# Performance work log

Hardware: AMD Instinct MI355X
Metric: run time of the kernel (lower is better)

Reference implementation:

```python
import jax, jax.numpy as jnp
import numpy as np

B, DEC, ENC, H = 4, 128, 512, 768


def setup_inputs() -> dict:
    key = jax.random.key(0)
    k1, k2, k3, k4, k5 = jax.random.split(key, 5)
    scale = 1.0 / np.sqrt(H)
    return {
        "decoder_state": jax.random.normal(k1, (B, DEC, H), dtype=jnp.float32),
        "encoder_outputs": jax.random.normal(k2, (B, ENC, H), dtype=jnp.float32),
        "mask": jnp.zeros((B, DEC, ENC), dtype=jnp.float32),
        # Learned params: torch nn.Linear(H, H, bias=False) weights, stored as (in, out)
        "W1": jax.random.normal(k3, (H, H), dtype=jnp.float32) * scale,
        "W2": jax.random.normal(k4, (H, H), dtype=jnp.float32) * scale,
        "vt": jax.random.normal(k5, (H,), dtype=jnp.float32) * scale,
    }


def reference(decoder_state, encoder_outputs, mask, W1, W2, vt):
    # enc_t: (B, enc, H), dec_t: (B, dec, H)
    enc_t = jnp.einsum("beh,hk->bek", encoder_outputs, W1)
    dec_t = jnp.einsum("bdh,hk->bdk", decoder_state, W2)
    # Bahdanau additive score: tanh of broadcast sum -> (B, dec, enc, H), reduce with vt
    hidden = jnp.tanh(enc_t[:, None, :, :] + dec_t[:, :, None, :])
    log_score = jnp.einsum("bdek,k->bde", hidden, vt)
    log_score_masked = log_score + mask
    return (log_score_masked, log_score)
```

## Files before the change

kernel.cpp:

```cpp
#include <hip/hip_runtime.h>
#include <hip/hip_bf16.h>

#define B_SZ   4
#define DEC_SZ 128
#define ENC_SZ 512
#define H_SZ   768
#define OUT_N  (B_SZ * DEC_SZ * ENC_SZ)

typedef __attribute__((ext_vector_type(8))) short s8v;
typedef __attribute__((ext_vector_type(4))) float fvec4;

__device__ inline unsigned short f2bf(float x) {
  union { float f; unsigned u; } v; v.f = x;
  unsigned r = v.u + 0x7FFF + ((v.u >> 16) & 1);
  return (unsigned short)(r >> 16);
}

__global__ __launch_bounds__(256) void transpose_w(const float* __restrict__ W1,
                                                   const float* __restrict__ W2,
                                                   unsigned short* __restrict__ T1,
                                                   unsigned short* __restrict__ T2) {
  const float* W = blockIdx.z ? W2 : W1;
  unsigned short* T = blockIdx.z ? T2 : T1;
  __shared__ float tile[64][65];
  int c0 = blockIdx.x * 64;
  int r0 = blockIdx.y * 64;
  int tx = threadIdx.x & 63, ty = threadIdx.x >> 6;
#pragma unroll
  for (int i = 0; i < 16; ++i) {
    int r = ty + i * 4;
    tile[r][tx] = W[(size_t)(r0 + r) * H_SZ + c0 + tx];
  }
  __syncthreads();
#pragma unroll
  for (int i = 0; i < 16; ++i) {
    int c = ty + i * 4;
    T[(size_t)(c0 + c) * H_SZ + r0 + tx] = f2bf(tile[tx][c]);
  }
}

__global__ __launch_bounds__(256) void cast_bf16(const float* __restrict__ enc,
                                                 const float* __restrict__ dec,
                                                 unsigned short* __restrict__ encB,
                                                 unsigned short* __restrict__ decB) {
  const float* x = blockIdx.z ? dec : enc;
  unsigned short* y = blockIdx.z ? decB : encB;
  int n4 = blockIdx.z ? (B_SZ * DEC_SZ * H_SZ / 4) : (B_SZ * ENC_SZ * H_SZ / 4);
  int i = blockIdx.x * 256 + threadIdx.x;
  if (i >= n4) return;
  float4 v = ((const float4*)x)[i];
  ushort4 o;
  o.x = f2bf(v.x); o.y = f2bf(v.y); o.z = f2bf(v.z); o.w = f2bf(v.w);
  ((ushort4*)y)[i] = o;
}

template <int TM, bool TILED>
__global__ __launch_bounds__(256) void gemm_nt_exp(const unsigned short* __restrict__ A,
                                                   const unsigned short* __restrict__ Bm,
                                                   float* __restrict__ C, int ldc) {
  const int m0 = blockIdx.x * TM;
  const int n0 = blockIdx.y * 64;

  __shared__ unsigned short As[TM][40];
  __shared__ unsigned short Bs[64][40];

  const int tid  = threadIdx.x;
  const int wave = tid >> 6;
  const int lane = tid & 63;
  const int l16  = lane & 15;
  const int quad = lane >> 4;
  const int MI   = TM / 64;
  const int wm   = wave * (TM / 4);

  const int ASEG = TM * 4 / 256;
  int ar[2], ak[2];
#pragma unroll
  for (int i = 0; i < ASEG; ++i) {
    int seg = tid + 256 * i;
    ar[i] = seg >> 2; ak[i] = (seg & 3) * 8;
  }
  const int br = tid >> 2, bk = (tid & 3) * 8;

  fvec4 acc[2][4];
#pragma unroll
  for (int i = 0; i < 2; ++i)
#pragma unroll
    for (int j = 0; j < 4; ++j) acc[i][j] = (fvec4)0.f;

  s8v pa[2], pb;
#pragma unroll
  for (int i = 0; i < ASEG; ++i)
    pa[i] = *(const s8v*)(A + (size_t)(m0 + ar[i]) * H_SZ + ak[i]);
  pb = *(const s8v*)(Bm + (size_t)(n0 + br) * H_SZ + bk);

  for (int k0 = 0; k0 < H_SZ; k0 += 32) {
    __syncthreads();
#pragma unroll
    for (int i = 0; i < ASEG; ++i) *(s8v*)&As[ar[i]][ak[i]] = pa[i];
    *(s8v*)&Bs[br][bk] = pb;
    __syncthreads();

    if (k0 + 32 < H_SZ) {
#pragma unroll
      for (int i = 0; i < ASEG; ++i)
        pa[i] = *(const s8v*)(A + (size_t)(m0 + ar[i]) * H_SZ + k0 + 32 + ak[i]);
      pb = *(const s8v*)(Bm + (size_t)(n0 + br) * H_SZ + k0 + 32 + bk);
    }

    s8v af[2], bf[4];
#pragma unroll
    for (int i = 0; i < MI; ++i) af[i] = *(const s8v*)&As[wm + i * 16 + l16][quad * 8];
#pragma unroll
    for (int j = 0; j < 4; ++j) bf[j] = *(const s8v*)&Bs[j * 16 + l16][quad * 8];
#pragma unroll
    for (int i = 0; i < MI; ++i)
#pragma unroll
      for (int j = 0; j < 4; ++j)
        acc[i][j] = __builtin_amdgcn_mfma_f32_16x16x32_bf16(af[i], bf[j], acc[i][j], 0, 0, 0);
  }

  const float C2 = 2.885390082f;
#pragma unroll
  for (int i = 0; i < MI; ++i) {
    int mbase = m0 + wm + i * 16 + quad * 4;
#pragma unroll
    for (int j = 0; j < 4; ++j) {
      int n = n0 + j * 16 + l16;
      if (TILED) {
        float4 o;
        o.x = __builtin_amdgcn_exp2f(acc[i][j][0] * C2);
        o.y = __builtin_amdgcn_exp2f(acc[i][j][1] * C2);
        o.z = __builtin_amdgcn_exp2f(acc[i][j][2] * C2);
        o.w = __builtin_amdgcn_exp2f(acc[i][j][3] * C2);
        int bIdx = n >> 9, es = (n >> 6) & 7, el = n & 63;
        ((float4*)C)[((size_t)(bIdx * 8 + es) * 192 + (mbase >> 2)) * 64 + el] = o;
      } else {
#pragma unroll
        for (int r = 0; r < 4; ++r)
          C[(size_t)(mbase + r) * ldc + n] = __builtin_amdgcn_exp2f(acc[i][j][r] * C2);
      }
    }
  }
}

__global__ __launch_bounds__(256) void score_out(const float* __restrict__ peT,
                                                 const float* __restrict__ pdm,
                                                 const float* __restrict__ vt,
                                                 const float* __restrict__ mask,
                                                 float* __restrict__ out) {
  const int tid  = threadIdx.x;
  const int wave = tid >> 6;
  const int lane = tid & 63;
  const int es   = blockIdx.x;
  const int d0   = blockIdx.y * 8;
  const int b    = blockIdx.z;

  __shared__ float pd_s[8][776];
  __shared__ float vts[768];

  {
    const int d = tid >> 5, l = tid & 31;
    const float* row = pdm + (size_t)(b * DEC_SZ + d0 + d) * H_SZ;
#pragma unroll
    for (int i = 0; i < 6; ++i)
      *(float4*)&pd_s[d][l * 4 + i * 128] = *(const float4*)(row + l * 4 + i * 128);
  }
  if (tid < 192) *(float4*)&vts[tid * 4] = *(const float4*)(vt + tid * 4);
  __syncthreads();

  float sumv = 0.f;
#pragma unroll
  for (int j = 0; j < 12; ++j) sumv += vts[lane + 64 * j];
#pragma unroll
  for (int s = 1; s < 64; s <<= 1) sumv += __shfl_xor(sumv, s, 64);

  float t0 = 0.f, t1 = 0.f;
  const float4* pe4 = (const float4*)peT + (size_t)(b * 8 + es) * 192 * 64 + lane;

  float4 buf[4];
#pragma unroll
  for (int i = 0; i < 4; ++i) buf[i] = pe4[(size_t)i * 64];

#pragma unroll 4
  for (int c = 0; c < 192; ++c) {
    float4 cur = buf[c & 3];
    if (c + 4 < 192) buf[c & 3] = pe4[(size_t)(c + 4) * 64];
    float4 v4 = *(const float4*)&vts[c * 4];
    float4 p0 = *(const float4*)&pd_s[wave * 2 + 0][c * 4];
    float4 p1 = *(const float4*)&pd_s[wave * 2 + 1][c * 4];
    t0 = fmaf(v4.x, __builtin_amdgcn_rcpf(fmaf(cur.x, p0.x, 1.f)), t0);
    t0 = fmaf(v4.y, __builtin_amdgcn_rcpf(fmaf(cur.y, p0.y, 1.f)), t0);
    t0 = fmaf(v4.z, __builtin_amdgcn_rcpf(fmaf(cur.z, p0.z, 1.f)), t0);
    t0 = fmaf(v4.w, __builtin_amdgcn_rcpf(fmaf(cur.w, p0.w, 1.f)), t0);
    t1 = fmaf(v4.x, __builtin_amdgcn_rcpf(fmaf(cur.x, p1.x, 1.f)), t1);
    t1 = fmaf(v4.y, __builtin_amdgcn_rcpf(fmaf(cur.y, p1.y, 1.f)), t1);
    t1 = fmaf(v4.z, __builtin_amdgcn_rcpf(fmaf(cur.z, p1.z, 1.f)), t1);
    t1 = fmaf(v4.w, __builtin_amdgcn_rcpf(fmaf(cur.w, p1.w, 1.f)), t1);
  }

  const int e = es * 64 + lane;
#pragma unroll
  for (int dd = 0; dd < 2; ++dd) {
    int d = d0 + wave * 2 + dd;
    size_t idx = ((size_t)(b * DEC_SZ + d)) * ENC_SZ + e;
    float s = fmaf(-2.f, dd ? t1 : t0, sumv);
    out[idx] = s + mask[idx];
    out[OUT_N + idx] = s;
  }
}

extern "C" void kernel_launch(void* const* d_in, const int* in_sizes, int n_in,
                              void* d_out, int out_size, void* d_ws, size_t ws_size,
                              hipStream_t stream) {
  (void)in_sizes; (void)n_in; (void)out_size; (void)ws_size;
  const float* dec  = (const float*)d_in[0];
  const float* enc  = (const float*)d_in[1];
  const float* mask = (const float*)d_in[2];
  const float* W1   = (const float*)d_in[3];
  const float* W2   = (const float*)d_in[4];
  const float* vt   = (const float*)d_in[5];
  float* out = (float*)d_out;

  float* peT = (float*)d_ws;
  float* pdm = peT + (size_t)H_SZ * B_SZ * ENC_SZ;
  unsigned short* W1T  = (unsigned short*)(pdm + (size_t)B_SZ * DEC_SZ * H_SZ);
  unsigned short* W2T  = W1T + (size_t)H_SZ * H_SZ;
  unsigned short* encB = W2T + (size_t)H_SZ * H_SZ;
  unsigned short* decB = encB + (size_t)B_SZ * ENC_SZ * H_SZ;

  transpose_w<<<dim3(12, 12, 2), 256, 0, stream>>>(W1, W2, W1T, W2T);
  cast_bf16<<<dim3(B_SZ * ENC_SZ * H_SZ / 4 / 256, 1, 2), 256, 0, stream>>>(
      enc, dec, encB, decB);

  gemm_nt_exp<128, true><<<dim3(H_SZ / 128, B_SZ * ENC_SZ / 64), 256, 0, stream>>>(
      W1T, encB, peT, 0);
  gemm_nt_exp<64, false><<<dim3(B_SZ * DEC_SZ / 64, H_SZ / 64), 256, 0, stream>>>(
      decB, W2T, pdm, H_SZ);

  score_out<<<dim3(ENC_SZ / 64, DEC_SZ / 8, B_SZ), 256, 0, stream>>>(
      peT, pdm, vt, mask, out);
}
```

Baseline: 142.5 us.

## Fuse bf16 casts into GEMM loads, merge both GEMMs, simplify score kernel

Removes the separate cast_bf16 kernel by converting fp32 encoder/decoder inputs to bf16 inside the GEMM global loads. Both projection GEMMs are merged into one launch with a block-index split, and the second GEMM now uses 128-row tiles. The score kernel drops LDS staging of the decoder row and vt, reading them directly from global memory (broadcast across the wave), handles one decoder row per wave, and deepens the peT prefetch to 8. This cuts launches and intermediate traffic, at the cost of more global reads per wave and less reuse of each peT load in the score loop.

```diff
diff --git a/kernel.cpp b/kernel.cpp
--- a/kernel.cpp
+++ b/kernel.cpp
@@ -14,6 +14,15 @@
   union { float f; unsigned u; } v; v.f = x;
   unsigned r = v.u + 0x7FFF + ((v.u >> 16) & 1);
   return (unsigned short)(r >> 16);
+}
+
+__device__ inline s8v load8(const unsigned short* p) { return *(const s8v*)p; }
+__device__ inline s8v load8(const float* p) {
+  float4 a = ((const float4*)p)[0];
+  float4 b = ((const float4*)p)[1];
+  unsigned short r[8] = {f2bf(a.x), f2bf(a.y), f2bf(a.z), f2bf(a.w),
+                         f2bf(b.x), f2bf(b.y), f2bf(b.z), f2bf(b.w)};
+  return *(const s8v*)r;
 }
 
 __global__ __launch_bounds__(256) void transpose_w(const float* __restrict__ W1,
@@ -39,29 +48,13 @@
   }
 }
 
-__global__ __launch_bounds__(256) void cast_bf16(const float* __restrict__ enc,
-                                                 const float* __restrict__ dec,
-                                                 unsigned short* __restrict__ encB,
-                                                 unsigned short* __restrict__ decB) {
-  const float* x = blockIdx.z ? dec : enc;
-  unsigned short* y = blockIdx.z ? decB : encB;
-  int n4 = blockIdx.z ? (B_SZ * DEC_SZ * H_SZ / 4) : (B_SZ * ENC_SZ * H_SZ / 4);
-  int i = blockIdx.x * 256 + threadIdx.x;
-  if (i >= n4) return;
-  float4 v = ((const float4*)x)[i];
-  ushort4 o;
-  o.x = f2bf(v.x); o.y = f2bf(v.y); o.z = f2bf(v.z); o.w = f2bf(v.w);
-  ((ushort4*)y)[i] = o;
-}
-
-template <int TM, bool TILED>
-__global__ __launch_bounds__(256) void gemm_nt_exp(const unsigned short* __restrict__ A,
-                                                   const unsigned short* __restrict__ Bm,
-                                                   float* __restrict__ C, int ldc) {
-  const int m0 = blockIdx.x * TM;
-  const int n0 = blockIdx.y * 64;
-
-  __shared__ unsigned short As[TM][40];
+template <bool TILED, typename TA, typename TB>
+__device__ inline void gemm_body(const TA* __restrict__ A, const TB* __restrict__ B,
+                                 float* __restrict__ C, int ldc, int bx, int by) {
+  const int m0 = bx * 128;
+  const int n0 = by * 64;
+
+  __shared__ unsigned short As[128][40];
   __shared__ unsigned short Bs[64][40];
 
   const int tid  = threadIdx.x;
@@ -69,13 +62,11 @@
   const int lane = tid & 63;
   const int l16  = lane & 15;
   const int quad = lane >> 4;
-  const int MI   = TM / 64;
-  const int wm   = wave * (TM / 4);
-
-  const int ASEG = TM * 4 / 256;
+  const int wm   = wave * 32;
+
   int ar[2], ak[2];
 #pragma unroll
-  for (int i = 0; i < ASEG; ++i) {
+  for (int i = 0; i < 2; ++i) {
     int seg = tid + 256 * i;
     ar[i] = seg >> 2; ak[i] = (seg & 3) * 8;
   }
@@ -89,31 +80,30 @@
 
   s8v pa[2], pb;
 #pragma unroll
-  for (int i = 0; i < ASEG; ++i)
-    pa[i] = *(const s8v*)(A + (size_t)(m0 + ar[i]) * H_SZ + ak[i]);
-  pb = *(const s8v*)(Bm + (size_t)(n0 + br) * H_SZ + bk);
+  for (int i = 0; i < 2; ++i) pa[i] = load8(A + (size_t)(m0 + ar[i]) * H_SZ + ak[i]);
+  pb = load8(B + (size_t)(n0 + br) * H_SZ + bk);
 
   for (int k0 = 0; k0 < H_SZ; k0 += 32) {
     __syncthreads();
 #pragma unroll
-    for (int i = 0; i < ASEG; ++i) *(s8v*)&As[ar[i]][ak[i]] = pa[i];
+    for (int i = 0; i < 2; ++i) *(s8v*)&As[ar[i]][ak[i]] = pa[i];
     *(s8v*)&Bs[br][bk] = pb;
     __syncthreads();
 
     if (k0 + 32 < H_SZ) {
 #pragma unroll
-      for (int i = 0; i < ASEG; ++i)
-        pa[i] = *(const s8v*)(A + (size_t)(m0 + ar[i]) * H_SZ + k0 + 32 + ak[i]);
-      pb = *(const s8v*)(Bm + (size_t)(n0 + br) * H_SZ + k0 + 32 + bk);
+      for (int i = 0; i < 2; ++i)
+        pa[i] = load8(A + (size_t)(m0 + ar[i]) * H_SZ + k0 + 32 + ak[i]);
+      pb = load8(B + (size_t)(n0 + br) * H_SZ + k0 + 32 + bk);
     }
 
     s8v af[2], bf[4];
 #pragma unroll
-    for (int i = 0; i < MI; ++i) af[i] = *(const s8v*)&As[wm + i * 16 + l16][quad * 8];
+    for (int i = 0; i < 2; ++i) af[i] = *(const s8v*)&As[wm + i * 16 + l16][quad * 8];
 #pragma unroll
     for (int j = 0; j < 4; ++j) bf[j] = *(const s8v*)&Bs[j * 16 + l16][quad * 8];
 #pragma unroll
-    for (int i = 0; i < MI; ++i)
+    for (int i = 0; i < 2; ++i)
 #pragma unroll
       for (int j = 0; j < 4; ++j)
         acc[i][j] = __builtin_amdgcn_mfma_f32_16x16x32_bf16(af[i], bf[j], acc[i][j], 0, 0, 0);
@@ -121,7 +111,7 @@
 
   const float C2 = 2.885390082f;
 #pragma unroll
-  for (int i = 0; i < MI; ++i) {
+  for (int i = 0; i < 2; ++i) {
     int mbase = m0 + wm + i * 16 + quad * 4;
 #pragma unroll
     for (int j = 0; j < 4; ++j) {
@@ -143,70 +133,64 @@
   }
 }
 
+__global__ __launch_bounds__(256) void gemm_both(const unsigned short* __restrict__ W1T,
+                                                 const float* __restrict__ enc,
+                                                 const float* __restrict__ dec,
+                                                 const unsigned short* __restrict__ W2T,
+                                                 float* __restrict__ peT,
+                                                 float* __restrict__ pdm) {
+  int bid = blockIdx.x;
+  if (bid < 192) {
+    gemm_body<true>(W1T, enc, peT, 0, bid % 6, bid / 6);
+  } else {
+    int r = bid - 192;
+    gemm_body<false>(dec, W2T, pdm, H_SZ, r % 4, r / 4);
+  }
+}
+
 __global__ __launch_bounds__(256) void score_out(const float* __restrict__ peT,
                                                  const float* __restrict__ pdm,
                                                  const float* __restrict__ vt,
                                                  const float* __restrict__ mask,
                                                  float* __restrict__ out) {
   const int tid  = threadIdx.x;
-  const int wave = tid >> 6;
   const int lane = tid & 63;
+  const int wave = __builtin_amdgcn_readfirstlane(tid >> 6);
   const int es   = blockIdx.x;
-  const int d0   = blockIdx.y * 8;
   const int b    = blockIdx.z;
-
-  __shared__ float pd_s[8][776];
-  __shared__ float vts[768];
-
-  {
-    const int d = tid >> 5, l = tid & 31;
-    const float* row = pdm + (size_t)(b * DEC_SZ + d0 + d) * H_SZ;
-#pragma unroll
-    for (int i = 0; i < 6; ++i)
-      *(float4*)&pd_s[d][l * 4 + i * 128] = *(const float4*)(row + l * 4 + i * 128);
-  }
-  if (tid < 192) *(float4*)&vts[tid * 4] = *(const float4*)(vt + tid * 4);
-  __syncthreads();
+  const int d    = blockIdx.y * 4 + wave;
 
   float sumv = 0.f;
 #pragma unroll
-  for (int j = 0; j < 12; ++j) sumv += vts[lane + 64 * j];
+  for (int j = 0; j < 12; ++j) sumv += vt[lane + 64 * j];
 #pragma unroll
   for (int s = 1; s < 64; s <<= 1) sumv += __shfl_xor(sumv, s, 64);
 
-  float t0 = 0.f, t1 = 0.f;
+  const float* pdrow = pdm + (size_t)(b * DEC_SZ + d) * H_SZ;
   const float4* pe4 = (const float4*)peT + (size_t)(b * 8 + es) * 192 * 64 + lane;
 
-  float4 buf[4];
-#pragma unroll
-  for (int i = 0; i < 4; ++i) buf[i] = pe4[(size_t)i * 64];
-
-#pragma unroll 4
+  float t0 = 0.f;
+  float4 buf[8];
+#pragma unroll
+  for (int i = 0; i < 8; ++i) buf[i] = pe4[(size_t)i * 64];
+
+#pragma unroll 8
   for (int c = 0; c < 192; ++c) {
-    float4 cur = buf[c & 3];
-    if (c + 4 < 192) buf[c & 3] = pe4[(size_t)(c + 4) * 64];
-    float4 v4 = *(const float4*)&vts[c * 4];
-    float4 p0 = *(const float4*)&pd_s[wave * 2 + 0][c * 4];
-    float4 p1 = *(const float4*)&pd_s[wave * 2 + 1][c * 4];
-    t0 = fmaf(v4.x, __builtin_amdgcn_rcpf(fmaf(cur.x, p0.x, 1.f)), t0);
-    t0 = fmaf(v4.y, __builtin_amdgcn_rcpf(fmaf(cur.y, p0.y, 1.f)), t0);
-    t0 = fmaf(v4.z, __builtin_amdgcn_rcpf(fmaf(cur.z, p0.z, 1.f)), t0);
-    t0 = fmaf(v4.w, __builtin_amdgcn_rcpf(fmaf(cur.w, p0.w, 1.f)), t0);
-    t1 = fmaf(v4.x, __builtin_amdgcn_rcpf(fmaf(cur.x, p1.x, 1.f)), t1);
-    t1 = fmaf(v4.y, __builtin_amdgcn_rcpf(fmaf(cur.y, p1.y, 1.f)), t1);
-    t1 = fmaf(v4.z, __builtin_amdgcn_rcpf(fmaf(cur.z, p1.z, 1.f)), t1);
-    t1 = fmaf(v4.w, __builtin_amdgcn_rcpf(fmaf(cur.w, p1.w, 1.f)), t1);
+    float4 cur = buf[c & 7];
+    if (c + 8 < 192) buf[c & 7] = pe4[(size_t)(c + 8) * 64];
+    float4 v4 = *(const float4*)(vt + c * 4);
+    float4 p4 = *(const float4*)(pdrow + c * 4);
+    t0 = fmaf(v4.x, __builtin_amdgcn_rcpf(fmaf(cur.x, p4.x, 1.f)), t0);
+    t0 = fmaf(v4.y, __builtin_amdgcn_rcpf(fmaf(cur.y, p4.y, 1.f)), t0);
+    t0 = fmaf(v4.z, __builtin_amdgcn_rcpf(fmaf(cur.z, p4.z, 1.f)), t0);
+    t0 = fmaf(v4.w, __builtin_amdgcn_rcpf(fmaf(cur.w, p4.w, 1.f)), t0);
   }
 
   const int e = es * 64 + lane;
-#pragma unroll
-  for (int dd = 0; dd < 2; ++dd) {
-    int d = d0 + wave * 2 + dd;
-    size_t idx = ((size_t)(b * DEC_SZ + d)) * ENC_SZ + e;
-    float s = fmaf(-2.f, dd ? t1 : t0, sumv);
-    out[idx] = s + mask[idx];
-    out[OUT_N + idx] = s;
-  }
+  size_t idx = ((size_t)(b * DEC_SZ + d)) * ENC_SZ + e;
+  float s = fmaf(-2.f, t0, sumv);
+  out[idx] = s + mask[idx];
+  out[OUT_N + idx] = s;
 }
 
 extern "C" void kernel_launch(void* const* d_in, const int* in_sizes, int n_in,
@@ -223,20 +207,11 @@
 
   float* peT = (float*)d_ws;
   float* pdm = peT + (size_t)H_SZ * B_SZ * ENC_SZ;
-  unsigned short* W1T  = (unsigned short*)(pdm + (size_t)B_SZ * DEC_SZ * H_SZ);
-  unsigned short* W2T  = W1T + (size_t)H_SZ * H_SZ;
-  unsigned short* encB = W2T + (size_t)H_SZ * H_SZ;
-  unsigned short* decB = encB + (size_t)B_SZ * ENC_SZ * H_SZ;
+  unsigned short* W1T = (unsigned short*)(pdm + (size_t)B_SZ * DEC_SZ * H_SZ);
+  unsigned short* W2T = W1T + (size_t)H_SZ * H_SZ;
 
   transpose_w<<<dim3(12, 12, 2), 256, 0, stream>>>(W1, W2, W1T, W2T);
-  cast_bf16<<<dim3(B_SZ * ENC_SZ * H_SZ / 4 / 256, 1, 2), 256, 0, stream>>>(
-      enc, dec, encB, decB);
-
-  gemm_nt_exp<128, true><<<dim3(H_SZ / 128, B_SZ * ENC_SZ / 64), 256, 0, stream>>>(
-      W1T, encB, peT, 0);
-  gemm_nt_exp<64, false><<<dim3(B_SZ * DEC_SZ / 64, H_SZ / 64), 256, 0, stream>>>(
-      decB, W2T, pdm, H_SZ);
-
-  score_out<<<dim3(ENC_SZ / 64, DEC_SZ / 8, B_SZ), 256, 0, stream>>>(
+  gemm_both<<<dim3(240), 256, 0, stream>>>(W1T, enc, dec, W2T, peT, pdm);
+  score_out<<<dim3(ENC_SZ / 64, DEC_SZ / 4, B_SZ), 256, 0, stream>>>(
       peT, pdm, vt, mask, out);
 }
```

Measured after the change: 133.2 us. 6.5% less time.
